# Kernel optimization log

Measured on AMD Instinct MI355X. Metric: run time of the kernel, lower is better.

Reference implementation:

```python
import jax, jax.numpy as jnp
import numpy as np

N = 131072   # total utterances (nodes)
B = 2048     # conversations (segments)
F = 200      # n_features (hard-coded 200 in source)
STEPS = 3    # processing_steps (reason_steps[0])


def setup_inputs() -> dict:
    key = jax.random.key(0)
    k = jax.random.split(key, 8)
    x = jax.random.normal(k[0], (N, F), dtype=jnp.float32)
    batch = jnp.sort(jax.random.randint(k[1], (N,), 0, B, dtype=jnp.int32))
    cos_coef = jax.random.normal(k[2], (N,), dtype=jnp.float32)
    q_star = jax.random.normal(k[3], (B, 2 * F), dtype=jnp.float32)
    s = 1.0 / np.sqrt(F)
    # PyTorch LSTM params: gate order i, f, g, o; input size 2F, hidden F
    W_ih = jax.random.uniform(k[4], (4 * F, 2 * F), jnp.float32, -s, s)
    W_hh = jax.random.uniform(k[5], (4 * F, F), jnp.float32, -s, s)
    b_ih = jax.random.uniform(k[6], (4 * F,), jnp.float32, -s, s)
    b_hh = jax.random.uniform(k[7], (4 * F,), jnp.float32, -s, s)
    return {"x": x, "batch": batch, "cos_coef": cos_coef, "q_star": q_star,
            "W_ih": W_ih, "W_hh": W_hh, "b_ih": b_ih, "b_hh": b_hh}


def _lstm_cell(inp, h, c, W_ih, W_hh, b_ih, b_hh):
    gates = inp @ W_ih.T + b_ih + h @ W_hh.T + b_hh  # [B, 4F]
    i, f, g, o = jnp.split(gates, 4, axis=-1)
    c = jax.nn.sigmoid(f) * c + jax.nn.sigmoid(i) * jnp.tanh(g)
    h = jax.nn.sigmoid(o) * jnp.tanh(c)
    return h, c


def reference(x, batch, cos_coef, q_star, W_ih, W_hh, b_ih, b_hh):
    # initial LSTM hidden: a_sit[i] = cos_row_i @ x[segment_i]  -> segment_sum
    h = jax.ops.segment_sum(cos_coef[:, None] * x, batch, num_segments=B)  # [B,F]
    c = jnp.zeros((B, F), dtype=x.dtype)
    for _ in range(STEPS):
        h, c = _lstm_cell(q_star, h, c, W_ih, W_hh, b_ih, b_hh)
        q = h                                            # [B,F]
        e = jnp.sum(x * q[batch], axis=-1)               # [N]
        m = jax.ops.segment_max(e, batch, num_segments=B)
        ex = jnp.exp(e - m[batch])
        denom = jax.ops.segment_sum(ex, batch, num_segments=B)
        a = ex / denom[batch]                            # per-segment softmax
        r = jax.ops.segment_sum(a[:, None] * x, batch, num_segments=B)  # [B,F]
        q_star = jnp.concatenate([q, r], axis=-1)        # [B,2F]
    return q_star
```

## Files before the change

### kernel.cpp

```cpp
#include <hip/hip_runtime.h>
#include <hip/hip_bf16.h>

#define N_NODES 131072
#define B_SEG   2048
#define F_DIM   200
#define K_DIM   608
#define NEG_INF (-3.4e38f)

typedef __attribute__((ext_vector_type(8))) short bf16x8;
typedef __attribute__((ext_vector_type(4))) float f32x4;

__device__ __forceinline__ float b2f(unsigned short u) {
  union { unsigned int i; float f; } v; v.i = ((unsigned int)u) << 16; return v.f;
}
__device__ __forceinline__ unsigned short f2bu(float f) {
  __hip_bfloat16 h = __float2bfloat16(f);
  return *reinterpret_cast<unsigned short*>(&h);
}
__device__ __forceinline__ float sigmoidf_(float x) { return 1.f / (1.f + __expf(-x)); }
__device__ __forceinline__ float tanhf_(float x) {
  float e = __expf(2.f * x);
  return 1.f - 2.f / (1.f + e);
}
__device__ __forceinline__ int lower_bound_batch(const int* __restrict__ batch, int target) {
  int lo = 0, hi = N_NODES;
  while (lo < hi) {
    int mid = (lo + hi) >> 1;
    if (batch[mid] < target) lo = mid + 1; else hi = mid;
  }
  return lo;
}

__global__ __launch_bounds__(256) void init_kernel(
    const float* __restrict__ xf, const int* __restrict__ batch,
    const float* __restrict__ cosc, const float* __restrict__ qs0,
    const float* __restrict__ Wih, const float* __restrict__ Whh,
    const float* __restrict__ bih, const float* __restrict__ bhh,
    unsigned short* __restrict__ xb, unsigned short* __restrict__ A,
    unsigned short* __restrict__ Wc, float* __restrict__ bsum,
    int* __restrict__ seg_off) {
  __shared__ float rpart[5][F_DIM];
  __shared__ int sb[2];
  int b = blockIdx.x, tid = threadIdx.x;
  if (tid < 2) sb[tid] = lower_bound_batch(batch, b + tid);
  int idx = b * 256 + tid;
  if (idx < 832 * K_DIM) {
    int row = idx / K_DIM, k = idx - row * K_DIM;
    float v = 0.f;
    if (row < 800) {
      if (k < 400)      v = Wih[row * 400 + k];
      else if (k < 600) v = Whh[row * 200 + (k - 400)];
    }
    Wc[idx] = f2bu(v);
  }
  if (idx < 800) bsum[idx] = bih[idx] + bhh[idx];
  __syncthreads();
  int start = sb[0], end = sb[1];
  int n = end - start;
  if (tid == 0) {
    seg_off[b] = start;
    if (b == 0) seg_off[B_SEG] = N_NODES;
  }
  unsigned short* Arow = A + (size_t)b * K_DIM;
  int rgrp = tid / 50, col4 = tid - rgrp * 50;
  float a0 = 0.f, a1 = 0.f, a2 = 0.f, a3 = 0.f;
  if (rgrp < 5) {
    for (int r = rgrp; r < n; r += 5) {
      float4 v = *(const float4*)(xf + (size_t)(start + r) * F_DIM + 4 * col4);
      ushort4 o; o.x = f2bu(v.x); o.y = f2bu(v.y); o.z = f2bu(v.z); o.w = f2bu(v.w);
      *(ushort4*)(xb + (size_t)(start + r) * F_DIM + 4 * col4) = o;
      float cv = cosc[start + r];
      a0 += cv * b2f(o.x); a1 += cv * b2f(o.y);
      a2 += cv * b2f(o.z); a3 += cv * b2f(o.w);
    }
    rpart[rgrp][4 * col4]     = a0;
    rpart[rgrp][4 * col4 + 1] = a1;
    rpart[rgrp][4 * col4 + 2] = a2;
    rpart[rgrp][4 * col4 + 3] = a3;
  }
  if (tid < 100) {
    float4 v = *(const float4*)(qs0 + (size_t)b * 400 + 4 * tid);
    ushort4 o; o.x = f2bu(v.x); o.y = f2bu(v.y); o.z = f2bu(v.z); o.w = f2bu(v.w);
    *(ushort4*)(Arow + 4 * tid) = o;
  }
  if (tid < 8) Arow[600 + tid] = 0;
  __syncthreads();
  if (tid < F_DIM) {
    float acc = rpart[0][tid] + rpart[1][tid] + rpart[2][tid] + rpart[3][tid]
              + rpart[4][tid];
    Arow[400 + tid] = f2bu(acc);
  }
}

__global__ __launch_bounds__(256) void gemm_gates(
    const unsigned short* __restrict__ A, const unsigned short* __restrict__ W,
    float* __restrict__ gates) {
  int tid = threadIdx.x;
  int bm = blockIdx.x * 32, bn = blockIdx.y * 64;
  int wave = tid >> 6, lane = tid & 63;
  int quad = lane >> 4, col = lane & 15;
  int strip = wave >> 1;
  int tp = (wave & 1) * 2;
  f32x4 acc[2];
  acc[0] = (f32x4){0.f, 0.f, 0.f, 0.f};
  acc[1] = (f32x4){0.f, 0.f, 0.f, 0.f};
  const unsigned short* Ap = A + (size_t)(bm + strip * 16 + col) * K_DIM + quad * 8;
  const unsigned short* Wp = W + (size_t)(bn + col) * K_DIM + quad * 8;
#pragma unroll
  for (int k0 = 0; k0 < K_DIM; k0 += 32) {
    bf16x8 af = *(const bf16x8*)(Ap + k0);
#pragma unroll
    for (int t = 0; t < 2; t++) {
      bf16x8 bfr = *(const bf16x8*)(Wp + (size_t)(tp + t) * 16 * K_DIM + k0);
      acc[t] = __builtin_amdgcn_mfma_f32_16x16x32_bf16(af, bfr, acc[t], 0, 0, 0);
    }
  }
#pragma unroll
  for (int t = 0; t < 2; t++) {
    int gn = bn + (tp + t) * 16 + col;
    if (gn < 800) {
#pragma unroll
      for (int r = 0; r < 4; r++) {
        int gm = bm + strip * 16 + quad * 4 + r;
        gates[(size_t)gm * 800 + gn] = acc[t][r];
      }
    }
  }
}

__global__ __launch_bounds__(256) void attn_fused(
    const unsigned short* __restrict__ xb, const int* __restrict__ seg_off,
    const float* __restrict__ gates, const float* __restrict__ bsum,
    float* __restrict__ cvec, unsigned short* __restrict__ A,
    float* __restrict__ out, int step) {
  __shared__ float q_s[F_DIM];
  __shared__ float rpart[8][F_DIM];
  __shared__ float redm[8], redl[8];
  int b = blockIdx.x, tid = threadIdx.x;
  int start = seg_off[b], end = seg_off[b + 1];
  int n = end - start;
  unsigned short* Arow = A + (size_t)b * K_DIM;
  if (tid < F_DIM) {
    int f = tid;
    const float* g = gates + (size_t)b * 800;
    float gi = g[f]       + bsum[f];
    float gf = g[200 + f] + bsum[200 + f];
    float gg = g[400 + f] + bsum[400 + f];
    float go = g[600 + f] + bsum[600 + f];
    float cp = (step > 0) ? cvec[(size_t)b * F_DIM + f] : 0.f;
    float cn = sigmoidf_(gf) * cp + sigmoidf_(gi) * tanhf_(gg);
    float hn = sigmoidf_(go) * tanhf_(cn);
    cvec[(size_t)b * F_DIM + f] = cn;
    q_s[f] = hn;
    if (step < 2) {
      unsigned short hb = f2bu(hn);
      Arow[f] = hb;
      Arow[400 + f] = hb;
    }
  }
  __syncthreads();
  int wave = tid >> 6, lane = tid & 63;
  int half = lane >> 5, hl = lane & 31;
  int hw = wave * 2 + half;
  bool act = (hl < 25);
  float q0=0,q1=0,q2=0,q3=0,q4=0,q5=0,q6=0,q7=0;
  if (act) {
    q0 = q_s[8*hl];   q1 = q_s[8*hl+1]; q2 = q_s[8*hl+2]; q3 = q_s[8*hl+3];
    q4 = q_s[8*hl+4]; q5 = q_s[8*hl+5]; q6 = q_s[8*hl+6]; q7 = q_s[8*hl+7];
  }
  const unsigned short* xp = xb + (size_t)start * F_DIM + 8 * hl;
  float m = NEG_INF, l = 0.f;
  float a0=0,a1=0,a2=0,a3=0,a4=0,a5=0,a6=0,a7=0;
  int r = hw;
  uint4 v = {0u, 0u, 0u, 0u};
  if (act && r < n) v = *(const uint4*)(xp + (size_t)r * F_DIM);
  for (; r < n; r += 8) {
    uint4 vc = v;
    int rn = r + 8;
    if (act && rn < n) v = *(const uint4*)(xp + (size_t)rn * F_DIM);
    float x0 = b2f((unsigned short)(vc.x & 0xffff)), x1 = b2f((unsigned short)(vc.x >> 16));
    float x2 = b2f((unsigned short)(vc.y & 0xffff)), x3 = b2f((unsigned short)(vc.y >> 16));
    float x4 = b2f((unsigned short)(vc.z & 0xffff)), x5 = b2f((unsigned short)(vc.z >> 16));
    float x6 = b2f((unsigned short)(vc.w & 0xffff)), x7 = b2f((unsigned short)(vc.w >> 16));
    float p = act ? (q0*x0 + q1*x1 + q2*x2 + q3*x3 + q4*x4 + q5*x5 + q6*x6 + q7*x7) : 0.f;
#pragma unroll
    for (int off = 16; off; off >>= 1) p += __shfl_xor(p, off, 32);
    float e = p;
    float mn = fmaxf(m, e);
    float fac = __expf(m - mn);
    float w  = __expf(e - mn);
    l  = l * fac + w;
    a0 = a0*fac + w*x0; a1 = a1*fac + w*x1; a2 = a2*fac + w*x2; a3 = a3*fac + w*x3;
    a4 = a4*fac + w*x4; a5 = a5*fac + w*x5; a6 = a6*fac + w*x6; a7 = a7*fac + w*x7;
    m = mn;
  }
  if (hl == 0) redm[hw] = m;
  __syncthreads();
  float M = fmaxf(fmaxf(fmaxf(redm[0], redm[1]), fmaxf(redm[2], redm[3])),
                  fmaxf(fmaxf(redm[4], redm[5]), fmaxf(redm[6], redm[7])));
  float facw = (m > NEG_INF) ? __expf(m - M) : 0.f;
  if (hl == 0) redl[hw] = l * facw;
  if (act) {
    float* rp = &rpart[hw][8 * hl];
    rp[0] = a0*facw; rp[1] = a1*facw; rp[2] = a2*facw; rp[3] = a3*facw;
    rp[4] = a4*facw; rp[5] = a5*facw; rp[6] = a6*facw; rp[7] = a7*facw;
  }
  __syncthreads();
  float L = redl[0]+redl[1]+redl[2]+redl[3]+redl[4]+redl[5]+redl[6]+redl[7];
  float inv = (L > 0.f) ? 1.f / L : 0.f;
  if (tid < F_DIM) {
    float rv = (rpart[0][tid]+rpart[1][tid]+rpart[2][tid]+rpart[3][tid]
              + rpart[4][tid]+rpart[5][tid]+rpart[6][tid]+rpart[7][tid]) * inv;
    if (step < 2) {
      Arow[200 + tid] = f2bu(rv);
    } else {
      out[(size_t)b * 400 + tid]       = q_s[tid];
      out[(size_t)b * 400 + 200 + tid] = rv;
    }
  }
}

extern "C" void kernel_launch(void* const* d_in, const int* in_sizes, int n_in,
                              void* d_out, int out_size, void* d_ws, size_t ws_size,
                              hipStream_t stream) {
  const float* x    = (const float*)d_in[0];
  const int*   batch= (const int*)d_in[1];
  const float* cosc = (const float*)d_in[2];
  const float* qs0  = (const float*)d_in[3];
  const float* Wih  = (const float*)d_in[4];
  const float* Whh  = (const float*)d_in[5];
  const float* bih  = (const float*)d_in[6];
  const float* bhh  = (const float*)d_in[7];
  char* ws = (char*)d_ws;
  unsigned short* xb   = (unsigned short*)(ws);
  unsigned short* A    = (unsigned short*)(ws + 52428800);
  unsigned short* Wc   = (unsigned short*)(ws + 54919168);
  float*          gates= (float*)(ws + 55930880);
  float*          cvec = (float*)(ws + 62484480);
  float*          bsum = (float*)(ws + 64122880);
  int*            soff = (int*)(ws + 64126080);
  float*          outp = (float*)d_out;

  init_kernel<<<B_SEG, 256, 0, stream>>>(x, batch, cosc, qs0, Wih, Whh, bih, bhh,
                                         xb, A, Wc, bsum, soff);
  for (int s = 0; s < 3; s++) {
    gemm_gates<<<dim3(64, 13), 256, 0, stream>>>(A, Wc, gates);
    attn_fused<<<B_SEG, 256, 0, stream>>>(xb, soff, gates, bsum, cvec, A, outp, s);
  }
}
```

Baseline: 274.0 us.

## Unroll online-softmax loop by two rows and prefetch in init segment sum

The attention loop now handles two rows per half-wave per iteration, with two outstanding loads, interleaved shuffle reductions and the running-max rescale skipped when the max does not change. The init kernel stages cosine coefficients in shared memory, software-prefetches the next x row, and accumulates with fp32 x instead of the bf16-rounded value. The last LSTM step no longer writes the cell state. A segment-length cap of 512 (NMAX) is added to the init kernel, which would silently truncate larger segments and exists only to size the shared buffer.

```diff
diff --git a/kernel.cpp b/kernel.cpp
--- a/kernel.cpp
+++ b/kernel.cpp
@@ -6,6 +6,7 @@
 #define F_DIM   200
 #define K_DIM   608
 #define NEG_INF (-3.4e38f)
+#define NMAX    512
 
 typedef __attribute__((ext_vector_type(8))) short bf16x8;
 typedef __attribute__((ext_vector_type(4))) float f32x4;
@@ -40,6 +41,7 @@
     unsigned short* __restrict__ Wc, float* __restrict__ bsum,
     int* __restrict__ seg_off) {
   __shared__ float rpart[5][F_DIM];
+  __shared__ float cw[NMAX];
   __shared__ int sb[2];
   int b = blockIdx.x, tid = threadIdx.x;
   if (tid < 2) sb[tid] = lower_bound_batch(batch, b + tid);
@@ -56,22 +58,31 @@
   if (idx < 800) bsum[idx] = bih[idx] + bhh[idx];
   __syncthreads();
   int start = sb[0], end = sb[1];
-  int n = end - start;
+  int n = end - start; if (n > NMAX) n = NMAX;
   if (tid == 0) {
     seg_off[b] = start;
     if (b == 0) seg_off[B_SEG] = N_NODES;
   }
+  for (int r = tid; r < n; r += 256) cw[r] = cosc[start + r];
+  __syncthreads();
   unsigned short* Arow = A + (size_t)b * K_DIM;
   int rgrp = tid / 50, col4 = tid - rgrp * 50;
   float a0 = 0.f, a1 = 0.f, a2 = 0.f, a3 = 0.f;
   if (rgrp < 5) {
-    for (int r = rgrp; r < n; r += 5) {
-      float4 v = *(const float4*)(xf + (size_t)(start + r) * F_DIM + 4 * col4);
-      ushort4 o; o.x = f2bu(v.x); o.y = f2bu(v.y); o.z = f2bu(v.z); o.w = f2bu(v.w);
-      *(ushort4*)(xb + (size_t)(start + r) * F_DIM + 4 * col4) = o;
-      float cv = cosc[start + r];
-      a0 += cv * b2f(o.x); a1 += cv * b2f(o.y);
-      a2 += cv * b2f(o.z); a3 += cv * b2f(o.w);
+    const float* xp = xf + (size_t)start * F_DIM + 4 * col4;
+    unsigned short* xw = xb + (size_t)start * F_DIM + 4 * col4;
+    int r = rgrp;
+    float4 v = {0.f, 0.f, 0.f, 0.f};
+    if (r < n) v = *(const float4*)(xp + (size_t)r * F_DIM);
+    for (; r < n; r += 5) {
+      float4 vc = v;
+      int rn = r + 5;
+      if (rn < n) v = *(const float4*)(xp + (size_t)rn * F_DIM);
+      ushort4 o;
+      o.x = f2bu(vc.x); o.y = f2bu(vc.y); o.z = f2bu(vc.z); o.w = f2bu(vc.w);
+      *(ushort4*)(xw + (size_t)r * F_DIM) = o;
+      float cv = cw[r];
+      a0 += cv * vc.x; a1 += cv * vc.y; a2 += cv * vc.z; a3 += cv * vc.w;
     }
     rpart[rgrp][4 * col4]     = a0;
     rpart[rgrp][4 * col4 + 1] = a1;
@@ -150,7 +161,7 @@
     float cp = (step > 0) ? cvec[(size_t)b * F_DIM + f] : 0.f;
     float cn = sigmoidf_(gf) * cp + sigmoidf_(gi) * tanhf_(gg);
     float hn = sigmoidf_(go) * tanhf_(cn);
-    cvec[(size_t)b * F_DIM + f] = cn;
+    if (step < 2) cvec[(size_t)b * F_DIM + f] = cn;
     q_s[f] = hn;
     if (step < 2) {
       unsigned short hb = f2bu(hn);
@@ -172,27 +183,47 @@
   float m = NEG_INF, l = 0.f;
   float a0=0,a1=0,a2=0,a3=0,a4=0,a5=0,a6=0,a7=0;
   int r = hw;
-  uint4 v = {0u, 0u, 0u, 0u};
-  if (act && r < n) v = *(const uint4*)(xp + (size_t)r * F_DIM);
-  for (; r < n; r += 8) {
-    uint4 vc = v;
-    int rn = r + 8;
-    if (act && rn < n) v = *(const uint4*)(xp + (size_t)rn * F_DIM);
-    float x0 = b2f((unsigned short)(vc.x & 0xffff)), x1 = b2f((unsigned short)(vc.x >> 16));
-    float x2 = b2f((unsigned short)(vc.y & 0xffff)), x3 = b2f((unsigned short)(vc.y >> 16));
-    float x4 = b2f((unsigned short)(vc.z & 0xffff)), x5 = b2f((unsigned short)(vc.z >> 16));
-    float x6 = b2f((unsigned short)(vc.w & 0xffff)), x7 = b2f((unsigned short)(vc.w >> 16));
-    float p = act ? (q0*x0 + q1*x1 + q2*x2 + q3*x3 + q4*x4 + q5*x5 + q6*x6 + q7*x7) : 0.f;
-#pragma unroll
-    for (int off = 16; off; off >>= 1) p += __shfl_xor(p, off, 32);
-    float e = p;
-    float mn = fmaxf(m, e);
-    float fac = __expf(m - mn);
-    float w  = __expf(e - mn);
-    l  = l * fac + w;
-    a0 = a0*fac + w*x0; a1 = a1*fac + w*x1; a2 = a2*fac + w*x2; a3 = a3*fac + w*x3;
-    a4 = a4*fac + w*x4; a5 = a5*fac + w*x5; a6 = a6*fac + w*x6; a7 = a7*fac + w*x7;
-    m = mn;
+  uint4 v1 = {0u,0u,0u,0u}, v2 = {0u,0u,0u,0u};
+  if (act && r < n)     v1 = *(const uint4*)(xp + (size_t)r * F_DIM);
+  if (act && r + 8 < n) v2 = *(const uint4*)(xp + (size_t)(r + 8) * F_DIM);
+  for (; r < n; r += 16) {
+    uint4 c1 = v1, c2 = v2;
+    bool has2 = (r + 8) < n;
+    int rn = r + 16;
+    if (act && rn < n)     v1 = *(const uint4*)(xp + (size_t)rn * F_DIM);
+    if (act && rn + 8 < n) v2 = *(const uint4*)(xp + (size_t)(rn + 8) * F_DIM);
+    float x10 = b2f((unsigned short)(c1.x & 0xffff)), x11 = b2f((unsigned short)(c1.x >> 16));
+    float x12 = b2f((unsigned short)(c1.y & 0xffff)), x13 = b2f((unsigned short)(c1.y >> 16));
+    float x14 = b2f((unsigned short)(c1.z & 0xffff)), x15 = b2f((unsigned short)(c1.z >> 16));
+    float x16 = b2f((unsigned short)(c1.w & 0xffff)), x17 = b2f((unsigned short)(c1.w >> 16));
+    float x20 = b2f((unsigned short)(c2.x & 0xffff)), x21 = b2f((unsigned short)(c2.x >> 16));
+    float x22 = b2f((unsigned short)(c2.y & 0xffff)), x23 = b2f((unsigned short)(c2.y >> 16));
+    float x24 = b2f((unsigned short)(c2.z & 0xffff)), x25 = b2f((unsigned short)(c2.z >> 16));
+    float x26 = b2f((unsigned short)(c2.w & 0xffff)), x27 = b2f((unsigned short)(c2.w >> 16));
+    float p1 = q0*x10 + q1*x11 + q2*x12 + q3*x13 + q4*x14 + q5*x15 + q6*x16 + q7*x17;
+    float p2 = q0*x20 + q1*x21 + q2*x22 + q3*x23 + q4*x24 + q5*x25 + q6*x26 + q7*x27;
+#pragma unroll
+    for (int off = 16; off; off >>= 1) {
+      p1 += __shfl_xor(p1, off, 32);
+      p2 += __shfl_xor(p2, off, 32);
+    }
+    float e1 = p1;
+    float e2 = has2 ? p2 : NEG_INF;
+    float mn = fmaxf(m, fmaxf(e1, e2));
+    float w1 = __expf(e1 - mn);
+    float w2 = __expf(e2 - mn);
+    if (mn > m) {
+      float fac = __expf(m - mn);
+      l *= fac;
+      a0 *= fac; a1 *= fac; a2 *= fac; a3 *= fac;
+      a4 *= fac; a5 *= fac; a6 *= fac; a7 *= fac;
+      m = mn;
+    }
+    l += w1 + w2;
+    a0 += w1*x10 + w2*x20; a1 += w1*x11 + w2*x21;
+    a2 += w1*x12 + w2*x22; a3 += w1*x13 + w2*x23;
+    a4 += w1*x14 + w2*x24; a5 += w1*x15 + w2*x25;
+    a6 += w1*x16 + w2*x26; a7 += w1*x17 + w2*x27;
   }
   if (hl == 0) redm[hw] = m;
   __syncthreads();
```

Measured after the change: 276.1 us. Within noise of the previous version (+0.8%).
